# Performance work log

Hardware: AMD Instinct MI355X
Metric: run time of the kernel (lower is better)

Reference implementation:

```python
import jax, jax.numpy as jnp
import numpy as np

LENGTHSCALES = np.array([0.1, 0.2, 0.5, 1.0, 2.0, 5.0, 10.0, 20.0], dtype=np.float32)
VALUE_DIM = 64
OUTPUT_DIM = 512
NUM_HEADS = len(LENGTHSCALES)


def setup_inputs() -> dict:
    key = jax.random.key(0)
    k1, k2, k3, k4, k5 = jax.random.split(key, 5)
    B, Lq, Lk, D = 4, 2048, 2048, 3
    query_positions = jax.random.normal(k1, (B, Lq, D), dtype=jnp.float32)
    key_positions = jax.random.normal(k2, (B, Lk, D), dtype=jnp.float32)
    values = jax.random.normal(k3, (B, Lk, NUM_HEADS, VALUE_DIM), dtype=jnp.float32)
    masked_elements = jax.random.randint(k4, (B, Lk), 0, 2) > 0
    # nn.Linear(value_dim*num_heads, output_dim, bias=False): weight [out, in]
    fan_in = VALUE_DIM * NUM_HEADS
    w_out = jax.random.uniform(k5, (OUTPUT_DIM, fan_in), dtype=jnp.float32,
                               minval=-1.0, maxval=1.0) / jnp.sqrt(fan_in)
    lengthscales = jnp.asarray(LENGTHSCALES)
    return {"query_positions": query_positions, "key_positions": key_positions,
            "values": values, "masked_elements": masked_elements,
            "lengthscales": lengthscales, "w_out": w_out}


def reference(query_positions, key_positions, values, masked_elements, lengthscales, w_out):
    # Euclidean distances via mm-trick (matches torch.cdist use_mm_for_euclid_dist)
    q2 = jnp.sum(query_positions ** 2, axis=-1)            # [B, Lq]
    k2 = jnp.sum(key_positions ** 2, axis=-1)              # [B, Lk]
    qk = jnp.einsum('bqd,bkd->bqk', query_positions, key_positions)
    d2 = jnp.maximum(q2[:, :, None] + k2[:, None, :] - 2.0 * qk, 0.0)
    distances = jnp.sqrt(d2)                               # [B, Lq, Lk]
    # per-head scaling + gaussian basis: exp(-(d/ls)^2)
    scaled = distances[:, None, :, :] / lengthscales[None, :, None, None]  # [B, H, Lq, Lk]
    scores = jnp.exp(-(scaled ** 2))
    scores = jnp.where(masked_elements[:, None, None, :], 0.0, scores)
    # masked sum-normalization
    scores = scores / (jnp.sum(jnp.abs(scores), axis=-1, keepdims=True) + 1e-5)
    # attend: values [B, Lk, H, V] -> [B, H, Lk, V]; then flatten heads -> [B, Lq, H*V]
    attended = jnp.einsum('bhqk,bkhv->bqhv', scores, values)
    B, Lq = attended.shape[0], attended.shape[1]
    flat = attended.reshape(B, Lq, -1)
    return flat @ w_out.T                                   # [B, Lq, output_dim]
```

## Files before the change

### kernel.cpp

```cpp
#include <hip/hip_runtime.h>
#include <math.h>

#define BB   4
#define LQ   2048
#define LK   2048
#define HD   8
#define VD   64
#define HV   512
#define OUTD 512
#define SP   72

typedef __attribute__((ext_vector_type(8))) short  bf16x8;
typedef __attribute__((ext_vector_type(4))) float  f32x4;

static __device__ __forceinline__ unsigned short f2bf(float f) {
    unsigned u = __builtin_bit_cast(unsigned, f);
    unsigned r = (u + 0x7fffu + ((u >> 16) & 1u)) >> 16;
    return (unsigned short)r;
}

__global__ __launch_bounds__(256) void cvt_vals(
    const float* __restrict__ vals, unsigned short* __restrict__ vals_t)
{
    __shared__ unsigned short st[64 * SP];
    const int tid = threadIdx.x;
    const int kt = blockIdx.x, h = blockIdx.y, b = blockIdx.z;

    const int k  = tid >> 2;
    const int vb = (tid & 3) * 16;
    const float* src = vals + (((size_t)(b * LK + kt * 64 + k) * HD + h)) * VD + vb;
    float4 f0 = *(const float4*)(src);
    float4 f1 = *(const float4*)(src + 4);
    float4 f2 = *(const float4*)(src + 8);
    float4 f3 = *(const float4*)(src + 12);
    const float fv[16] = {f0.x,f0.y,f0.z,f0.w, f1.x,f1.y,f1.z,f1.w,
                          f2.x,f2.y,f2.z,f2.w, f3.x,f3.y,f3.z,f3.w};
#pragma unroll
    for (int j = 0; j < 16; ++j) st[(vb + j) * SP + k] = f2bf(fv[j]);
    __syncthreads();

    const int v  = tid >> 2;
    const int kb = (tid & 3) * 16;
    uint4 o0 = *(const uint4*)&st[v * SP + kb];
    uint4 o1 = *(const uint4*)&st[v * SP + kb + 8];
    unsigned short* dst = vals_t + ((size_t)((b * HD + h) * VD + v)) * LK + kt * 64 + kb;
    *(uint4*)dst       = o0;
    *(uint4*)(dst + 8) = o1;
}

__global__ __launch_bounds__(256) void attend2(
    const float* __restrict__ qpos,
    const float* __restrict__ kpos,
    const unsigned short* __restrict__ vals_t,
    const int*   __restrict__ kmask,
    const float* __restrict__ ls,
    unsigned short* __restrict__ attended)
{
    __shared__ unsigned short sS[64 * SP];
    __shared__ unsigned short sV[64 * SP];
    __shared__ float s_kx[64], s_ky[64], s_kz[64];
    __shared__ float s_pd[256];
    __shared__ float s_inv[64];

    const int tid = threadIdx.x;
    const int qt = blockIdx.x, h = blockIdx.y, b = blockIdx.z;
    const int q0 = qt * 64;

    const float lsh  = ls[h];
    const float negc = -1.0f / (lsh * lsh);

    const int sq = tid >> 2;
    const int so = tid & 3;
    const float* qp = qpos + (size_t)(b * LQ + q0 + sq) * 3;
    const float qx = qp[0], qy = qp[1], qz = qp[2];

    const int vv = tid >> 3;
    const int vc = tid & 7;
    const unsigned short* vt_base = vals_t + (size_t)((b * HD + h) * VD) * LK;

    const int wave = tid >> 6;
    const int lane = tid & 63;
    const int ln = lane & 15, kq = lane >> 4;

    float pden = 0.f;
    f32x4 acc[4];
#pragma unroll
    for (int n = 0; n < 4; ++n) acc[n] = (f32x4){0.f, 0.f, 0.f, 0.f};

    for (int kt = 0; kt < LK; kt += 64) {
        __syncthreads();
        if (tid < 64) {
            const float* kp = kpos + (size_t)(b * LK + kt + tid) * 3;
            const int m = kmask[b * LK + kt + tid];
            float kx = kp[0];
            if (m) kx = 3.0e37f;
            s_kx[tid] = kx; s_ky[tid] = kp[1]; s_kz[tid] = kp[2];
        }
        {
            const unsigned short* src = vt_base + (size_t)vv * LK + kt + vc * 8;
            uint4 d0 = *(const uint4*)src;
            uint4 d1 = *(const uint4*)(src + (size_t)32 * LK);
            *(uint4*)&sV[vv * SP + vc * 8]        = d0;
            *(uint4*)&sV[(vv + 32) * SP + vc * 8] = d1;
        }
        __syncthreads();

#pragma unroll
        for (int p = 0; p < 2; ++p) {
            const int o = so + 4 * p;
            float kxa[8], kya[8], kza[8];
            *(float4*)&kxa[0] = *(const float4*)&s_kx[o * 8];
            *(float4*)&kxa[4] = *(const float4*)&s_kx[o * 8 + 4];
            *(float4*)&kya[0] = *(const float4*)&s_ky[o * 8];
            *(float4*)&kya[4] = *(const float4*)&s_ky[o * 8 + 4];
            *(float4*)&kza[0] = *(const float4*)&s_kz[o * 8];
            *(float4*)&kza[4] = *(const float4*)&s_kz[o * 8 + 4];
            unsigned pk[4];
            unsigned short us[8];
#pragma unroll
            for (int j = 0; j < 8; ++j) {
                const float dx = qx - kxa[j];
                const float dy = qy - kya[j];
                const float dz = qz - kza[j];
                const float d2 = fmaf(dx, dx, fmaf(dy, dy, dz * dz));
                const float sc = __expf(d2 * negc);
                pden += sc;
                us[j] = f2bf(sc);
            }
#pragma unroll
            for (int j = 0; j < 4; ++j)
                pk[j] = (unsigned)us[2 * j] | ((unsigned)us[2 * j + 1] << 16);
            *(uint4*)&sS[sq * SP + o * 8] = make_uint4(pk[0], pk[1], pk[2], pk[3]);
        }
        __syncthreads();

        {
            const unsigned short* ap = &sS[(wave * 16 + ln) * SP + kq * 8];
            const bf16x8 a0 = *(const bf16x8*)(ap);
            const bf16x8 a1 = *(const bf16x8*)(ap + 32);
#pragma unroll
            for (int n = 0; n < 4; ++n) {
                const unsigned short* bp = &sV[(n * 16 + ln) * SP + kq * 8];
                const bf16x8 b0 = *(const bf16x8*)(bp);
                const bf16x8 b1 = *(const bf16x8*)(bp + 32);
                acc[n] = __builtin_amdgcn_mfma_f32_16x16x32_bf16(a0, b0, acc[n], 0, 0, 0);
                acc[n] = __builtin_amdgcn_mfma_f32_16x16x32_bf16(a1, b1, acc[n], 0, 0, 0);
            }
        }
    }

    s_pd[tid] = pden;
    __syncthreads();
    if (tid < 64) {
        const float d = s_pd[tid * 4] + s_pd[tid * 4 + 1] +
                        s_pd[tid * 4 + 2] + s_pd[tid * 4 + 3];
        s_inv[tid] = 1.0f / (d + 1e-5f);
    }
    __syncthreads();

#pragma unroll
    for (int n = 0; n < 4; ++n) {
#pragma unroll
        for (int r = 0; r < 4; ++r) {
            const int q = wave * 16 + kq * 4 + r;
            const float val = acc[n][r] * s_inv[q];
            attended[(size_t)(b * LQ + q0 + q) * HV + h * VD + n * 16 + ln] = f2bf(val);
        }
    }
}

__global__ __launch_bounds__(256) void proj2(
    const unsigned short* __restrict__ A,
    const float* __restrict__ W,
    float* __restrict__ C)
{
    __shared__ unsigned short sA[64 * SP];
    __shared__ unsigned short sW[64 * SP];

    const int tid = threadIdx.x;
    const int n0 = blockIdx.x * 64, m0 = blockIdx.y * 64;
    const int wave = tid >> 6, lane = tid & 63;
    const int ln = lane & 15, kq = lane >> 4;

    const int am = tid >> 3, ac = tid & 7;
    const int wn = tid >> 2, wk = (tid & 3) * 16;

    f32x4 acc[4];
#pragma unroll
    for (int n = 0; n < 4; ++n) acc[n] = (f32x4){0.f, 0.f, 0.f, 0.f};

    for (int k0 = 0; k0 < 512; k0 += 64) {
        __syncthreads();
        {
            const unsigned short* asrc = A + (size_t)(m0 + am) * 512 + k0 + ac * 8;
            uint4 a0 = *(const uint4*)asrc;
            uint4 a1 = *(const uint4*)(asrc + (size_t)32 * 512);
            *(uint4*)&sA[am * SP + ac * 8]        = a0;
            *(uint4*)&sA[(am + 32) * SP + ac * 8] = a1;
        }
        {
            const float* wsrc = W + (size_t)(n0 + wn) * 512 + k0 + wk;
            float4 w0 = *(const float4*)(wsrc);
            float4 w1 = *(const float4*)(wsrc + 4);
            float4 w2 = *(const float4*)(wsrc + 8);
            float4 w3 = *(const float4*)(wsrc + 12);
            const float wf[16] = {w0.x,w0.y,w0.z,w0.w, w1.x,w1.y,w1.z,w1.w,
                                  w2.x,w2.y,w2.z,w2.w, w3.x,w3.y,w3.z,w3.w};
            unsigned pk[8];
#pragma unroll
            for (int j = 0; j < 8; ++j)
                pk[j] = (unsigned)f2bf(wf[2 * j]) | ((unsigned)f2bf(wf[2 * j + 1]) << 16);
            *(uint4*)&sW[wn * SP + wk]     = make_uint4(pk[0], pk[1], pk[2], pk[3]);
            *(uint4*)&sW[wn * SP + wk + 8] = make_uint4(pk[4], pk[5], pk[6], pk[7]);
        }
        __syncthreads();

        const unsigned short* ap = &sA[(wave * 16 + ln) * SP + kq * 8];
        const bf16x8 a0 = *(const bf16x8*)(ap);
        const bf16x8 a1 = *(const bf16x8*)(ap + 32);
#pragma unroll
        for (int n = 0; n < 4; ++n) {
            const unsigned short* bp = &sW[(n * 16 + ln) * SP + kq * 8];
            const bf16x8 b0 = *(const bf16x8*)(bp);
            const bf16x8 b1 = *(const bf16x8*)(bp + 32);
            acc[n] = __builtin_amdgcn_mfma_f32_16x16x32_bf16(a0, b0, acc[n], 0, 0, 0);
            acc[n] = __builtin_amdgcn_mfma_f32_16x16x32_bf16(a1, b1, acc[n], 0, 0, 0);
        }
    }

#pragma unroll
    for (int n = 0; n < 4; ++n) {
#pragma unroll
        for (int r = 0; r < 4; ++r) {
            C[(size_t)(m0 + wave * 16 + kq * 4 + r) * 512 + n0 + n * 16 + ln] = acc[n][r];
        }
    }
}

extern "C" void kernel_launch(void* const* d_in, const int* in_sizes, int n_in,
                              void* d_out, int out_size, void* d_ws, size_t ws_size,
                              hipStream_t stream) {
    const float* qpos  = (const float*)d_in[0];
    const float* kpos  = (const float*)d_in[1];
    const float* vals  = (const float*)d_in[2];
    const int*   kmask = (const int*)  d_in[3];
    const float* ls    = (const float*)d_in[4];
    const float* wout  = (const float*)d_in[5];
    float* out = (float*)d_out;

    unsigned short* vals_t   = (unsigned short*)d_ws;
    unsigned short* attended = vals_t + (size_t)4 * 1024 * 1024;

    cvt_vals<<<dim3(32, HD, BB), 256, 0, stream>>>(vals, vals_t);
    attend2 <<<dim3(32, HD, BB), 256, 0, stream>>>(qpos, kpos, vals_t, kmask, ls, attended);
    proj2   <<<dim3(OUTD / 64, (BB * LQ) / 64), 256, 0, stream>>>(attended, wout, out);
}
```

Measured before the change: 167.6 us.

## Compute scores in registers, share distances across head pairs, drop LDS staging

The attention kernel is restructured so that each 512-thread block handles 32 queries across all 8 heads. Each wave covers a 16-query strip for two heads and reuses one distance computation for both heads' exponentials. Score fragments are built directly in MFMA operand registers, and value fragments are loaded straight from global memory, which removes the shared-memory round trips and the three barriers per key tile. Key positions for the whole batch are staged once into LDS, and the row sums are reduced with wave shuffles. In exchange, values are now read uncoalesced from global memory per wave with no LDS sharing, and register pressure goes up.

```diff
diff --git a/kernel.cpp b/kernel.cpp
--- a/kernel.cpp
+++ b/kernel.cpp
@@ -12,6 +12,7 @@
 
 typedef __attribute__((ext_vector_type(8))) short  bf16x8;
 typedef __attribute__((ext_vector_type(4))) float  f32x4;
+typedef __attribute__((ext_vector_type(4))) unsigned int u32x4;
 
 static __device__ __forceinline__ unsigned short f2bf(float f) {
     unsigned u = __builtin_bit_cast(unsigned, f);
@@ -48,7 +49,7 @@
     *(uint4*)(dst + 8) = o1;
 }
 
-__global__ __launch_bounds__(256) void attend2(
+__global__ __launch_bounds__(512, 2) void attend3(
     const float* __restrict__ qpos,
     const float* __restrict__ kpos,
     const unsigned short* __restrict__ vals_t,
@@ -56,115 +57,128 @@
     const float* __restrict__ ls,
     unsigned short* __restrict__ attended)
 {
-    __shared__ unsigned short sS[64 * SP];
-    __shared__ unsigned short sV[64 * SP];
-    __shared__ float s_kx[64], s_ky[64], s_kz[64];
-    __shared__ float s_pd[256];
-    __shared__ float s_inv[64];
+    __shared__ __align__(16) float s_kx[LK];
+    __shared__ __align__(16) float s_ky[LK];
+    __shared__ __align__(16) float s_kz[LK];
 
     const int tid = threadIdx.x;
-    const int qt = blockIdx.x, h = blockIdx.y, b = blockIdx.z;
-    const int q0 = qt * 64;
-
-    const float lsh  = ls[h];
-    const float negc = -1.0f / (lsh * lsh);
-
-    const int sq = tid >> 2;
-    const int so = tid & 3;
-    const float* qp = qpos + (size_t)(b * LQ + q0 + sq) * 3;
+    const int qt = blockIdx.x, b = blockIdx.y;
+    const int q0 = qt * 32;
+
+    for (int i = tid; i < LK; i += 512) {
+        const float* kp = kpos + (size_t)(b * LK + i) * 3;
+        float kx = kp[0];
+        if (kmask[b * LK + i]) kx = 3.0e37f;
+        s_kx[i] = kx; s_ky[i] = kp[1]; s_kz[i] = kp[2];
+    }
+    __syncthreads();
+
+    const int wave  = tid >> 6;
+    const int lane  = tid & 63;
+    const int ln    = lane & 15;
+    const int kq    = lane >> 4;
+    const int strip = wave & 1;
+    const int h0    = (wave >> 1) * 2;
+
+    const int qrow = q0 + strip * 16 + ln;
+    const float* qp = qpos + (size_t)(b * LQ + qrow) * 3;
     const float qx = qp[0], qy = qp[1], qz = qp[2];
 
-    const int vv = tid >> 3;
-    const int vc = tid & 7;
-    const unsigned short* vt_base = vals_t + (size_t)((b * HD + h) * VD) * LK;
-
-    const int wave = tid >> 6;
-    const int lane = tid & 63;
-    const int ln = lane & 15, kq = lane >> 4;
-
-    float pden = 0.f;
-    f32x4 acc[4];
-#pragma unroll
-    for (int n = 0; n < 4; ++n) acc[n] = (f32x4){0.f, 0.f, 0.f, 0.f};
+    const float ls0 = ls[h0], ls1 = ls[h0 + 1];
+    const float negc0 = -1.0f / (ls0 * ls0);
+    const float negc1 = -1.0f / (ls1 * ls1);
+
+    const unsigned short* vt0 = vals_t + ((size_t)((b * HD + h0)     * VD) + ln) * LK + kq * 8;
+    const unsigned short* vt1 = vals_t + ((size_t)((b * HD + h0 + 1) * VD) + ln) * LK + kq * 8;
+
+    f32x4 acc0[4], acc1[4];
+#pragma unroll
+    for (int n = 0; n < 4; ++n) {
+        acc0[n] = (f32x4){0.f, 0.f, 0.f, 0.f};
+        acc1[n] = (f32x4){0.f, 0.f, 0.f, 0.f};
+    }
+    float pden0 = 0.f, pden1 = 0.f;
 
     for (int kt = 0; kt < LK; kt += 64) {
-        __syncthreads();
-        if (tid < 64) {
-            const float* kp = kpos + (size_t)(b * LK + kt + tid) * 3;
-            const int m = kmask[b * LK + kt + tid];
-            float kx = kp[0];
-            if (m) kx = 3.0e37f;
-            s_kx[tid] = kx; s_ky[tid] = kp[1]; s_kz[tid] = kp[2];
-        }
-        {
-            const unsigned short* src = vt_base + (size_t)vv * LK + kt + vc * 8;
-            uint4 d0 = *(const uint4*)src;
-            uint4 d1 = *(const uint4*)(src + (size_t)32 * LK);
-            *(uint4*)&sV[vv * SP + vc * 8]        = d0;
-            *(uint4*)&sV[(vv + 32) * SP + vc * 8] = d1;
-        }
-        __syncthreads();
-
-#pragma unroll
-        for (int p = 0; p < 2; ++p) {
-            const int o = so + 4 * p;
+        bf16x8 vf0[4][2], vf1[4][2];
+#pragma unroll
+        for (int n = 0; n < 4; ++n) {
+#pragma unroll
+            for (int s = 0; s < 2; ++s) {
+                vf0[n][s] = *(const bf16x8*)(vt0 + (size_t)n * 16 * LK + kt + s * 32);
+                vf1[n][s] = *(const bf16x8*)(vt1 + (size_t)n * 16 * LK + kt + s * 32);
+            }
+        }
+
+        bf16x8 a0[2], a1[2];
+#pragma unroll
+        for (int s = 0; s < 2; ++s) {
+            const int kb = kt + s * 32 + kq * 8;
             float kxa[8], kya[8], kza[8];
-            *(float4*)&kxa[0] = *(const float4*)&s_kx[o * 8];
-            *(float4*)&kxa[4] = *(const float4*)&s_kx[o * 8 + 4];
-            *(float4*)&kya[0] = *(const float4*)&s_ky[o * 8];
-            *(float4*)&kya[4] = *(const float4*)&s_ky[o * 8 + 4];
-            *(float4*)&kza[0] = *(const float4*)&s_kz[o * 8];
-            *(float4*)&kza[4] = *(const float4*)&s_kz[o * 8 + 4];
-            unsigned pk[4];
-            unsigned short us[8];
+            *(float4*)&kxa[0] = *(const float4*)&s_kx[kb];
+            *(float4*)&kxa[4] = *(const float4*)&s_kx[kb + 4];
+            *(float4*)&kya[0] = *(const float4*)&s_ky[kb];
+            *(float4*)&kya[4] = *(const float4*)&s_ky[kb + 4];
+            *(float4*)&kza[0] = *(const float4*)&s_kz[kb];
+            *(float4*)&kza[4] = *(const float4*)&s_kz[kb + 4];
+            float e0[8], e1[8];
 #pragma unroll
             for (int j = 0; j < 8; ++j) {
                 const float dx = qx - kxa[j];
                 const float dy = qy - kya[j];
                 const float dz = qz - kza[j];
                 const float d2 = fmaf(dx, dx, fmaf(dy, dy, dz * dz));
-                const float sc = __expf(d2 * negc);
-                pden += sc;
-                us[j] = f2bf(sc);
-            }
-#pragma unroll
-            for (int j = 0; j < 4; ++j)
-                pk[j] = (unsigned)us[2 * j] | ((unsigned)us[2 * j + 1] << 16);
-            *(uint4*)&sS[sq * SP + o * 8] = make_uint4(pk[0], pk[1], pk[2], pk[3]);
-        }
-        __syncthreads();
-
-        {
-            const unsigned short* ap = &sS[(wave * 16 + ln) * SP + kq * 8];
-            const bf16x8 a0 = *(const bf16x8*)(ap);
-            const bf16x8 a1 = *(const bf16x8*)(ap + 32);
+                e0[j] = __expf(d2 * negc0);
+                e1[j] = __expf(d2 * negc1);
+                pden0 += e0[j];
+                pden1 += e1[j];
+            }
+            unsigned short us0[8], us1[8];
+#pragma unroll
+            for (int j = 0; j < 8; ++j) {
+                us0[j] = f2bf(e0[j]);
+                us1[j] = f2bf(e1[j]);
+            }
+            u32x4 p0, p1;
+#pragma unroll
+            for (int j = 0; j < 4; ++j) {
+                p0[j] = (unsigned)us0[2 * j] | ((unsigned)us0[2 * j + 1] << 16);
+                p1[j] = (unsigned)us1[2 * j] | ((unsigned)us1[2 * j + 1] << 16);
+            }
+            a0[s] = __builtin_bit_cast(bf16x8, p0);
+            a1[s] = __builtin_bit_cast(bf16x8, p1);
+        }
+
+#pragma unroll
+        for (int s = 0; s < 2; ++s) {
 #pragma unroll
             for (int n = 0; n < 4; ++n) {
-                const unsigned short* bp = &sV[(n * 16 + ln) * SP + kq * 8];
-                const bf16x8 b0 = *(const bf16x8*)(bp);
-                const bf16x8 b1 = *(const bf16x8*)(bp + 32);
-                acc[n] = __builtin_amdgcn_mfma_f32_16x16x32_bf16(a0, b0, acc[n], 0, 0, 0);
-                acc[n] = __builtin_amdgcn_mfma_f32_16x16x32_bf16(a1, b1, acc[n], 0, 0, 0);
-            }
-        }
-    }
-
-    s_pd[tid] = pden;
-    __syncthreads();
-    if (tid < 64) {
-        const float d = s_pd[tid * 4] + s_pd[tid * 4 + 1] +
-                        s_pd[tid * 4 + 2] + s_pd[tid * 4 + 3];
-        s_inv[tid] = 1.0f / (d + 1e-5f);
-    }
-    __syncthreads();
-
+                acc0[n] = __builtin_amdgcn_mfma_f32_16x16x32_bf16(a0[s], vf0[n][s], acc0[n], 0, 0, 0);
+                acc1[n] = __builtin_amdgcn_mfma_f32_16x16x32_bf16(a1[s], vf1[n][s], acc1[n], 0, 0, 0);
+            }
+        }
+    }
+
+    pden0 += __shfl_xor(pden0, 16);
+    pden0 += __shfl_xor(pden0, 32);
+    pden1 += __shfl_xor(pden1, 16);
+    pden1 += __shfl_xor(pden1, 32);
+
+    f32x4 inv0, inv1;
+#pragma unroll
+    for (int r = 0; r < 4; ++r) {
+        inv0[r] = 1.0f / (__shfl(pden0, kq * 4 + r) + 1e-5f);
+        inv1[r] = 1.0f / (__shfl(pden1, kq * 4 + r) + 1e-5f);
+    }
+
+    unsigned short* op = attended
+        + (size_t)(b * LQ + q0 + strip * 16 + kq * 4) * HV + h0 * VD + ln;
 #pragma unroll
     for (int n = 0; n < 4; ++n) {
 #pragma unroll
         for (int r = 0; r < 4; ++r) {
-            const int q = wave * 16 + kq * 4 + r;
-            const float val = acc[n][r] * s_inv[q];
-            attended[(size_t)(b * LQ + q0 + q) * HV + h * VD + n * 16 + ln] = f2bf(val);
+            op[(size_t)r * HV + n * 16]      = f2bf(acc0[n][r] * inv0[r]);
+            op[(size_t)r * HV + VD + n * 16] = f2bf(acc1[n][r] * inv1[r]);
         }
     }
 }
@@ -252,6 +266,6 @@
     unsigned short* attended = vals_t + (size_t)4 * 1024 * 1024;
 
     cvt_vals<<<dim3(32, HD, BB), 256, 0, stream>>>(vals, vals_t);
-    attend2 <<<dim3(32, HD, BB), 256, 0, stream>>>(qpos, kpos, vals_t, kmask, ls, attended);
+    attend3 <<<dim3(LQ / 32, BB), 512, 0, stream>>>(qpos, kpos, vals_t, kmask, ls, attended);
     proj2   <<<dim3(OUTD / 64, (BB * LQ) / 64), 256, 0, stream>>>(attended, wout, out);
 }
```

Result: slower. 249.3 us (+48.7%).
